# Performance work log

Measured on AMD Instinct MI355X. Metric: run time of the kernel, lower is better.

The kernel has to match this reference:

```python
import jax, jax.numpy as jnp
import numpy as np

DECAY = 0.999


def setup_inputs() -> dict:
    key = jax.random.key(0)
    ks = jax.random.split(key, 10)
    B, S, H, P, N = 2, 8192, 2048, 512, 64
    return {
        "hidden_states": jax.random.normal(ks[0], (B, S, H), jnp.float32),
        "pred_state": jax.random.normal(ks[1], (P,), jnp.float32),
        "mem_states": jax.random.normal(ks[2], (N, H), jnp.float32),
        "mem_strength": jax.random.uniform(ks[3], (N,), jnp.float32),
        "W_ih": jax.random.normal(ks[4], (3 * P, H), jnp.float32) * 0.02,
        "W_hh": jax.random.normal(ks[5], (3 * P, P), jnp.float32) * 0.02,
        "b_ih": jax.random.normal(ks[6], (3 * P,), jnp.float32) * 0.02,
        "b_hh": jax.random.normal(ks[7], (3 * P,), jnp.float32) * 0.02,
        "pred_proj_w": jax.random.normal(ks[8], (H, P), jnp.float32) * 0.02,
        "input_proj_w": jax.random.normal(ks[9], (H, H), jnp.float32) * 0.02,
        "surprise_scale": jnp.float32(1.0),
        "write_ptr": 3,
    }


def gru_cell(x, h, W_ih, W_hh, b_ih, b_hh):
    # PyTorch GRUCell: gates ordered (reset, update, new)
    gi = W_ih @ x + b_ih
    gh = W_hh @ h + b_hh
    i_r, i_z, i_n = jnp.split(gi, 3)
    h_r, h_z, h_n = jnp.split(gh, 3)
    r = jax.nn.sigmoid(i_r + h_r)
    z = jax.nn.sigmoid(i_z + h_z)
    n = jnp.tanh(i_n + r * h_n)
    return (1.0 - z) * n + z * h


def reference(hidden_states, pred_state, mem_states, mem_strength,
              W_ih, W_hh, b_ih, b_hh, pred_proj_w, input_proj_w,
              surprise_scale, write_ptr):
    H = hidden_states.shape[-1]
    seq_len = hidden_states.shape[1]
    n_slots = mem_states.shape[0]

    actual = hidden_states.mean(axis=(0, 1))               # (H,) dominant reduction
    predicted = pred_proj_w @ pred_state                   # (H,)
    prediction_error = actual - predicted
    error_norm = jnp.linalg.norm(prediction_error) / (H ** 0.5)
    surprise = jax.nn.sigmoid(surprise_scale * error_norm)

    # decay + one-hot slot blend (== scatter-set at slot)
    mem_strength_new = mem_strength * (DECAY ** seq_len)
    slot = write_ptr % n_slots
    mem_states_new = mem_states.at[slot].set(actual * surprise)
    mem_strength_new = mem_strength_new.at[slot].set(surprise)

    # predictor update
    x_gru = input_proj_w @ actual
    new_pred_state = gru_cell(x_gru, pred_state, W_ih, W_hh, b_ih, b_hh)

    return (surprise, prediction_error, predicted,
            mem_states_new, mem_strength_new, new_pred_state)
```

## Files before the change

kernel.cpp:

```cpp
#include <hip/hip_runtime.h>
#include <math.h>

constexpr int Hc   = 2048;
constexpr int Pc   = 512;
constexpr int Nc   = 64;
constexpr int ROWS = 16384;
constexpr int SUMB = 512;
constexpr int ROWS_PER_B = ROWS / SUMB;

constexpr int O_SUR  = 0;
constexpr int O_PERR = 1;
constexpr int O_PRED = O_PERR + Hc;
constexpr int O_MEM  = O_PRED + Hc;
constexpr int O_MEMS = O_MEM + Nc * Hc;
constexpr int O_NPS  = O_MEMS + Nc;

constexpr size_t WS_PART = 0;
constexpr size_t WS_ACT  = (size_t)SUMB * Hc;
constexpr size_t WS_XGRU = WS_ACT + Hc;
constexpr size_t WS_GH   = WS_XGRU + Hc;
constexpr size_t WS_ERR2 = WS_GH + 1536;

__device__ __forceinline__ float warp_dot(const float* __restrict__ w,
                                          const float* __restrict__ x, int len) {
    int lane = threadIdx.x & 63;
    float s = 0.f;
    for (int i = lane * 4; i < len; i += 64 * 4) {
        float4 wv = *(const float4*)(w + i);
        float4 xv = *(const float4*)(x + i);
        s += wv.x * xv.x + wv.y * xv.y + wv.z * xv.z + wv.w * xv.w;
    }
    #pragma unroll
    for (int off = 32; off; off >>= 1) s += __shfl_xor(s, off);
    return s;
}

__global__ __launch_bounds__(256) void k1(const float* __restrict__ hs,
                                          const float* __restrict__ pred_state,
                                          const float* __restrict__ mem_states,
                                          const float* __restrict__ mem_strength,
                                          const float* __restrict__ W_hh,
                                          const float* __restrict__ pred_proj_w,
                                          float* __restrict__ out,
                                          float* __restrict__ ws) {
    const int bid = blockIdx.x, t = threadIdx.x;
    if (bid < SUMB) {
        float4 a0 = make_float4(0.f, 0.f, 0.f, 0.f);
        float4 a1 = make_float4(0.f, 0.f, 0.f, 0.f);
        const float* base = hs + (size_t)bid * ROWS_PER_B * Hc;
        for (int r = 0; r < ROWS_PER_B; ++r) {
            const float4* rp = (const float4*)(base + (size_t)r * Hc);
            float4 v0 = rp[t];
            float4 v1 = rp[t + 256];
            a0.x += v0.x; a0.y += v0.y; a0.z += v0.z; a0.w += v0.w;
            a1.x += v1.x; a1.y += v1.y; a1.z += v1.z; a1.w += v1.w;
        }
        float4* wp = (float4*)(ws + WS_PART + (size_t)bid * Hc);
        wp[t] = a0;
        wp[t + 256] = a1;
    } else if (bid < SUMB + 128) {
        int base_row = (bid - SUMB) * 16 + (t >> 6) * 4;
        #pragma unroll
        for (int rr = 0; rr < 4; ++rr) {
            int row = base_row + rr;
            float d = warp_dot(pred_proj_w + (size_t)row * Pc, pred_state, Pc);
            if ((t & 63) == 0) out[O_PRED + row] = d;
        }
    } else if (bid < SUMB + 224) {
        int base_row = (bid - (SUMB + 128)) * 16 + (t >> 6) * 4;
        #pragma unroll
        for (int rr = 0; rr < 4; ++rr) {
            int row = base_row + rr;
            float d = warp_dot(W_hh + (size_t)row * Pc, pred_state, Pc);
            if ((t & 63) == 0) ws[WS_GH + row] = d;
        }
    } else {
        int cb = bid - (SUMB + 224);
        #pragma unroll
        for (int i = 0; i < 16; ++i) {
            int idx = (cb * 16 + i) * 256 + t;
            out[O_MEM + idx] = mem_states[idx];
        }
        if (cb == 0 && t < Nc) {
            double ds = pow(0.999, 8192.0);
            out[O_MEMS + t] = mem_strength[t] * (float)ds;
        }
    }
}

__global__ __launch_bounds__(256) void k2(float* __restrict__ out,
                                          float* __restrict__ ws) {
    const int c = blockIdx.x * 256 + threadIdx.x;
    float s = 0.f;
    #pragma unroll 8
    for (int p = 0; p < SUMB; ++p) s += ws[WS_PART + (size_t)p * Hc + c];
    float actual = s * (1.0f / (float)ROWS);
    ws[WS_ACT + c] = actual;
    float pe = actual - out[O_PRED + c];
    out[O_PERR + c] = pe;
    float e2 = pe * pe;
    #pragma unroll
    for (int off = 32; off; off >>= 1) e2 += __shfl_xor(e2, off);
    __shared__ float sm[4];
    if ((threadIdx.x & 63) == 0) sm[threadIdx.x >> 6] = e2;
    __syncthreads();
    if (threadIdx.x == 0) ws[WS_ERR2 + blockIdx.x] = sm[0] + sm[1] + sm[2] + sm[3];
}

__global__ __launch_bounds__(256) void k3(const float* __restrict__ input_proj_w,
                                          const float* __restrict__ surprise_scale,
                                          const int* __restrict__ write_ptr,
                                          float* __restrict__ out,
                                          float* __restrict__ ws) {
    const int bid = blockIdx.x;
    if (bid < 512) {
        int row = bid * 4 + (threadIdx.x >> 6);
        float d = warp_dot(input_proj_w + (size_t)row * Hc, ws + WS_ACT, Hc);
        if ((threadIdx.x & 63) == 0) ws[WS_XGRU + row] = d;
    } else {
        __shared__ float s_sur;
        __shared__ int s_slot;
        if (threadIdx.x == 0) {
            float e2 = 0.f;
            #pragma unroll
            for (int i = 0; i < 8; ++i) e2 += ws[WS_ERR2 + i];
            float norm = sqrtf(e2 * (1.0f / (float)Hc));
            float sur = 1.f / (1.f + expf(-surprise_scale[0] * norm));
            out[O_SUR] = sur;
            int slot = write_ptr[0] % Nc;
            if (slot < 0) slot += Nc;
            out[O_MEMS + slot] = sur;
            s_sur = sur;
            s_slot = slot;
        }
        __syncthreads();
        float sur = s_sur;
        int slot = s_slot;
        for (int c = threadIdx.x; c < Hc; c += 256)
            out[O_MEM + (size_t)slot * Hc + c] = ws[WS_ACT + c] * sur;
    }
}

__global__ __launch_bounds__(256) void k4(const float* __restrict__ W_ih,
                                          const float* __restrict__ b_ih,
                                          const float* __restrict__ b_hh,
                                          const float* __restrict__ pred_state,
                                          float* __restrict__ out,
                                          float* __restrict__ ws) {
    const int k0 = blockIdx.x * 4;
    const int wave = threadIdx.x >> 6;
    __shared__ float gi_s[12];
    #pragma unroll
    for (int j = 0; j < 3; ++j) {
        int d = wave * 3 + j;
        int g = d >> 2, e = d & 3;
        int row = g * 512 + k0 + e;
        float v = warp_dot(W_ih + (size_t)row * Hc, ws + WS_XGRU, Hc);
        if ((threadIdx.x & 63) == 0) gi_s[d] = v;
    }
    __syncthreads();
    if (threadIdx.x < 4) {
        int k = k0 + threadIdx.x;
        float i_r = gi_s[threadIdx.x]     + b_ih[k];
        float i_z = gi_s[4 + threadIdx.x] + b_ih[512 + k];
        float i_n = gi_s[8 + threadIdx.x] + b_ih[1024 + k];
        float h_r = ws[WS_GH + k]        + b_hh[k];
        float h_z = ws[WS_GH + 512 + k]  + b_hh[512 + k];
        float h_n = ws[WS_GH + 1024 + k] + b_hh[1024 + k];
        float r = 1.f / (1.f + expf(-(i_r + h_r)));
        float z = 1.f / (1.f + expf(-(i_z + h_z)));
        float n = tanhf(i_n + r * h_n);
        float h = pred_state[k];
        out[O_NPS + k] = (1.f - z) * n + z * h;
    }
}

extern "C" void kernel_launch(void* const* d_in, const int* in_sizes, int n_in,
                              void* d_out, int out_size, void* d_ws, size_t ws_size,
                              hipStream_t stream) {
    const float* hs            = (const float*)d_in[0];
    const float* pred_state    = (const float*)d_in[1];
    const float* mem_states    = (const float*)d_in[2];
    const float* mem_strength  = (const float*)d_in[3];
    const float* W_ih          = (const float*)d_in[4];
    const float* W_hh          = (const float*)d_in[5];
    const float* b_ih          = (const float*)d_in[6];
    const float* b_hh          = (const float*)d_in[7];
    const float* pred_proj_w   = (const float*)d_in[8];
    const float* input_proj_w  = (const float*)d_in[9];
    const float* surprise_scale= (const float*)d_in[10];
    const int*   write_ptr     = (const int*)d_in[11];
    float* out = (float*)d_out;
    float* ws  = (float*)d_ws;

    k1<<<768, 256, 0, stream>>>(hs, pred_state, mem_states, mem_strength,
                                W_hh, pred_proj_w, out, ws);
    k2<<<8, 256, 0, stream>>>(out, ws);
    k3<<<513, 256, 0, stream>>>(input_proj_w, surprise_scale, write_ptr, out, ws);
    k4<<<128, 256, 0, stream>>>(W_ih, b_ih, b_hh, pred_state, out, ws);
}
```

Baseline: 274.4 us.

## Retile column-mean reduction into row-by-column chunks with in-block shuffle reduce

The hidden-state column sum is restructured from 512 blocks that each sum 32 full rows into 2048 blocks that each cover a 1024-row by 16-column tile. Each block reduces its tile with wave shuffles and shared memory, so only 16 partial rows reach the workspace and k2 reads 16 partials instead of 512. This cuts partial-sum traffic and k2 work and adds memory-level parallelism in k1. The cost is strided 64-byte row segments per wave, which may lower coalescing efficiency on the dominant 268 MB stream, plus a launch bound hint of 4 blocks per CU.

```diff
diff --git a/kernel.cpp b/kernel.cpp
--- a/kernel.cpp
+++ b/kernel.cpp
@@ -5,8 +5,16 @@
 constexpr int Pc   = 512;
 constexpr int Nc   = 64;
 constexpr int ROWS = 16384;
-constexpr int SUMB = 512;
-constexpr int ROWS_PER_B = ROWS / SUMB;
+
+constexpr int RCHUNKS = 16;
+constexpr int CCHUNKS = 128;
+constexpr int SUMB    = RCHUNKS * CCHUNKS;
+constexpr int ROWS_PER_CHUNK = ROWS / RCHUNKS;
+
+constexpr int B_PRED0 = SUMB;
+constexpr int B_GH0   = SUMB + 128;
+constexpr int B_CPY0  = SUMB + 224;
+constexpr int K1_GRID = SUMB + 256;
 
 constexpr int O_SUR  = 0;
 constexpr int O_PERR = 1;
@@ -16,7 +24,7 @@
 constexpr int O_NPS  = O_MEMS + Nc;
 
 constexpr size_t WS_PART = 0;
-constexpr size_t WS_ACT  = (size_t)SUMB * Hc;
+constexpr size_t WS_ACT  = (size_t)RCHUNKS * Hc;
 constexpr size_t WS_XGRU = WS_ACT + Hc;
 constexpr size_t WS_GH   = WS_XGRU + Hc;
 constexpr size_t WS_ERR2 = WS_GH + 1536;
@@ -35,39 +43,54 @@
     return s;
 }
 
-__global__ __launch_bounds__(256) void k1(const float* __restrict__ hs,
-                                          const float* __restrict__ pred_state,
-                                          const float* __restrict__ mem_states,
-                                          const float* __restrict__ mem_strength,
-                                          const float* __restrict__ W_hh,
-                                          const float* __restrict__ pred_proj_w,
-                                          float* __restrict__ out,
-                                          float* __restrict__ ws) {
+__global__ __launch_bounds__(256, 4) void k1(const float* __restrict__ hs,
+                                             const float* __restrict__ pred_state,
+                                             const float* __restrict__ mem_states,
+                                             const float* __restrict__ mem_strength,
+                                             const float* __restrict__ W_hh,
+                                             const float* __restrict__ pred_proj_w,
+                                             float* __restrict__ out,
+                                             float* __restrict__ ws) {
     const int bid = blockIdx.x, t = threadIdx.x;
     if (bid < SUMB) {
-        float4 a0 = make_float4(0.f, 0.f, 0.f, 0.f);
-        float4 a1 = make_float4(0.f, 0.f, 0.f, 0.f);
-        const float* base = hs + (size_t)bid * ROWS_PER_B * Hc;
-        for (int r = 0; r < ROWS_PER_B; ++r) {
-            const float4* rp = (const float4*)(base + (size_t)r * Hc);
-            float4 v0 = rp[t];
-            float4 v1 = rp[t + 256];
-            a0.x += v0.x; a0.y += v0.y; a0.z += v0.z; a0.w += v0.w;
-            a1.x += v1.x; a1.y += v1.y; a1.z += v1.z; a1.w += v1.w;
-        }
-        float4* wp = (float4*)(ws + WS_PART + (size_t)bid * Hc);
-        wp[t] = a0;
-        wp[t + 256] = a1;
-    } else if (bid < SUMB + 128) {
-        int base_row = (bid - SUMB) * 16 + (t >> 6) * 4;
+        const int rowchunk = bid >> 7;
+        const int colchunk = bid & 127;
+        const int cf = t & 3;
+        const int r0 = t >> 2;
+        const float* base = hs + (size_t)rowchunk * ROWS_PER_CHUNK * Hc
+                               + colchunk * 16 + cf * 4;
+        float4 acc = make_float4(0.f, 0.f, 0.f, 0.f);
+        #pragma unroll
+        for (int i = 0; i < 16; ++i) {
+            float4 v = *(const float4*)(base + (size_t)(r0 + 64 * i) * Hc);
+            acc.x += v.x; acc.y += v.y; acc.z += v.z; acc.w += v.w;
+        }
+        #pragma unroll
+        for (int off = 4; off <= 32; off <<= 1) {
+            acc.x += __shfl_xor(acc.x, off);
+            acc.y += __shfl_xor(acc.y, off);
+            acc.z += __shfl_xor(acc.z, off);
+            acc.w += __shfl_xor(acc.w, off);
+        }
+        __shared__ float4 sm[4][4];
+        if ((t & 63) < 4) sm[t >> 6][t & 3] = acc;
+        __syncthreads();
+        if (t < 4) {
+            float4 a = sm[0][t], b = sm[1][t], c = sm[2][t], d = sm[3][t];
+            float4 r = make_float4(a.x + b.x + c.x + d.x, a.y + b.y + c.y + d.y,
+                                   a.z + b.z + c.z + d.z, a.w + b.w + c.w + d.w);
+            *(float4*)(ws + WS_PART + (size_t)rowchunk * Hc + colchunk * 16 + t * 4) = r;
+        }
+    } else if (bid < B_GH0) {
+        int base_row = (bid - B_PRED0) * 16 + (t >> 6) * 4;
         #pragma unroll
         for (int rr = 0; rr < 4; ++rr) {
             int row = base_row + rr;
             float d = warp_dot(pred_proj_w + (size_t)row * Pc, pred_state, Pc);
             if ((t & 63) == 0) out[O_PRED + row] = d;
         }
-    } else if (bid < SUMB + 224) {
-        int base_row = (bid - (SUMB + 128)) * 16 + (t >> 6) * 4;
+    } else if (bid < B_CPY0) {
+        int base_row = (bid - B_GH0) * 16 + (t >> 6) * 4;
         #pragma unroll
         for (int rr = 0; rr < 4; ++rr) {
             int row = base_row + rr;
@@ -75,7 +98,7 @@
             if ((t & 63) == 0) ws[WS_GH + row] = d;
         }
     } else {
-        int cb = bid - (SUMB + 224);
+        int cb = bid - B_CPY0;
         #pragma unroll
         for (int i = 0; i < 16; ++i) {
             int idx = (cb * 16 + i) * 256 + t;
@@ -92,8 +115,8 @@
                                           float* __restrict__ ws) {
     const int c = blockIdx.x * 256 + threadIdx.x;
     float s = 0.f;
-    #pragma unroll 8
-    for (int p = 0; p < SUMB; ++p) s += ws[WS_PART + (size_t)p * Hc + c];
+    #pragma unroll
+    for (int p = 0; p < RCHUNKS; ++p) s += ws[WS_PART + (size_t)p * Hc + c];
     float actual = s * (1.0f / (float)ROWS);
     ws[WS_ACT + c] = actual;
     float pe = actual - out[O_PRED + c];
@@ -193,8 +216,8 @@
     float* out = (float*)d_out;
     float* ws  = (float*)d_ws;
 
-    k1<<<768, 256, 0, stream>>>(hs, pred_state, mem_states, mem_strength,
-                                W_hh, pred_proj_w, out, ws);
+    k1<<<K1_GRID, 256, 0, stream>>>(hs, pred_state, mem_states, mem_strength,
+                                    W_hh, pred_proj_w, out, ws);
     k2<<<8, 256, 0, stream>>>(out, ws);
     k3<<<513, 256, 0, stream>>>(input_proj_w, surprise_scale, write_ptr, out, ws);
     k4<<<128, 256, 0, stream>>>(W_ih, b_ih, b_hh, pred_state, out, ws);
```

Measured after the change: 263.9 us. 3.8% less time.
